# Optimization experiments

Hardware: AMD Instinct MI355X
Metric: run time of the kernel (lower is better)

Reference implementation:

```python
import jax, jax.numpy as jnp
import numpy as np

EPS = 1e-5  # BatchNorm eps (torch default)

def conv2d(x, w, padding=0, dilation=1):
    # x: NCHW, w: OIHW
    return jax.lax.conv_general_dilated(
        x, w, window_strides=(1, 1),
        padding=[(padding, padding), (padding, padding)],
        rhs_dilation=(dilation, dilation),
        dimension_numbers=('NCHW', 'OIHW', 'NCHW'))

def bn_relu(x, scale, bias):
    # eval-mode BatchNorm with running_mean=0, running_var=1, then ReLU
    inv = scale / np.sqrt(1.0 + EPS)
    return jax.nn.relu(x * inv[None, :, None, None] + bias[None, :, None, None])

def setup_inputs() -> dict:
    key = jax.random.key(0)
    ks = jax.random.split(key, 12)
    B, C, H, W = 4, 512, 64, 64
    def nrm(k, shape, fan):
        return jax.random.normal(k, shape, jnp.float32) * np.sqrt(2.0 / fan)
    return {
        'x': jax.random.normal(ks[0], (B, C, H, W), jnp.float32),
        'w_a1': nrm(ks[1], (128, 512, 1, 1), 1 * 1 * 128),
        'w_a2': nrm(ks[2], (128, 512, 3, 3), 3 * 3 * 128),
        'w_a3': nrm(ks[3], (128, 512, 3, 3), 3 * 3 * 128),
        'w_a4': nrm(ks[4], (128, 512, 3, 3), 3 * 3 * 128),
        'w_a5': nrm(ks[5], (128, 512, 1, 1), 1 * 1 * 128),
        'bn_scale': jnp.ones((5, 128), jnp.float32),
        'bn_bias': jnp.zeros((5, 128), jnp.float32),
        'w_q': jax.random.normal(ks[6], (128, 640, 1, 1), jnp.float32) * 0.04,
        'b_q': jnp.zeros((128,), jnp.float32),
        'w_k': jax.random.normal(ks[7], (128, 640, 1, 1), jnp.float32) * 0.04,
        'b_k': jnp.zeros((128,), jnp.float32),
        'w_v': jax.random.normal(ks[8], (512, 512, 1, 1), jnp.float32) * 0.04,
        'b_v': jnp.zeros((512,), jnp.float32),
        'gamma': jax.random.uniform(ks[9], (1,), jnp.float32),
    }

def reference(x, w_a1, w_a2, w_a3, w_a4, w_a5, bn_scale, bn_bias,
              w_q, b_q, w_k, b_k, w_v, b_v, gamma):
    B, C, H, W = x.shape
    N = H * W
    # ASPP branches (query and key paths use identical weights & input,
    # so compute once and reuse — same math as the original)
    b1 = bn_relu(conv2d(x, w_a1, 0, 1), bn_scale[0], bn_bias[0])
    b2 = bn_relu(conv2d(x, w_a2, 2, 2), bn_scale[1], bn_bias[1])
    b3 = bn_relu(conv2d(x, w_a3, 3, 3), bn_scale[2], bn_bias[2])
    b4 = bn_relu(conv2d(x, w_a4, 6, 6), bn_scale[3], bn_bias[3])
    # aspp5: global avg pool -> 1x1 conv -> BN -> ReLU -> bilinear up to HxW
    # (bilinear upsample of a 1x1 map with align_corners=True is a broadcast)
    p5 = jnp.mean(x, axis=(2, 3), keepdims=True)            # [B,512,1,1]
    p5 = bn_relu(conv2d(p5, w_a5, 0, 1), bn_scale[4], bn_bias[4])
    b5 = jnp.broadcast_to(p5, (B, 128, H, W))
    feat = jnp.concatenate([b1, b2, b3, b4, b5], axis=1)    # [B,640,H,W]

    q = (conv2d(feat, w_q) + b_q[None, :, None, None]).reshape(B, 128, N)  # [B,128,N]
    k = (conv2d(feat, w_k) + b_k[None, :, None, None]).reshape(B, 128, N)  # [B,128,N]
    v = (conv2d(x, w_v) + b_v[None, :, None, None]).reshape(B, C, N)       # [B,C,N]

    energy = jnp.einsum('bcn,bcm->bnm', q, k)               # [B,N,N], unscaled
    attention = jax.nn.softmax(energy, axis=-1)
    out = jnp.einsum('bcm,bnm->bcn', v, attention).reshape(B, C, H, W)
    return gamma[0] * out + x
```

## Files before the change

### kernel.cpp

```cpp
#include <hip/hip_runtime.h>

typedef _Float16 f16x8 __attribute__((ext_vector_type(8)));
typedef _Float16 f16x4 __attribute__((ext_vector_type(4)));
typedef float f32x4 __attribute__((ext_vector_type(4)));

#define N_PIX 4096
#define C_IN  512
#define BN_INV 0.99999500003749969f
#define CCH 64

#define GLOAD_LDS16(g, l)                                        \
  __builtin_amdgcn_global_load_lds(                              \
      (const __attribute__((address_space(1))) void*)(g),        \
      (__attribute__((address_space(3))) void*)(l), 16, 0, 0)

__device__ __forceinline__ f32x4 mfma16(f16x8 a, f16x8 b, f32x4 c) {
  return __builtin_amdgcn_mfma_f32_16x16x32_f16(a, b, c, 0, 0, 0);
}
__device__ __forceinline__ f16x8 ldnt(const _Float16* base, int row, int ld, int k0, int lane) {
  return *(const f16x8*)(base + (size_t)(row + (lane & 15)) * ld + k0 + ((lane >> 4) << 3));
}

__global__ __launch_bounds__(256) void k_xT(const float* __restrict__ x, _Float16* __restrict__ xT) {
  __shared__ float t[32][33];
  int b = blockIdx.z, p0 = blockIdx.x * 32, c0 = blockIdx.y * 32;
  int tx = threadIdx.x & 31, ty = threadIdx.x >> 5;
  const float* xb = x + ((size_t)b * C_IN + c0) * N_PIX + p0;
  for (int i = 0; i < 32; i += 8) t[ty + i][tx] = xb[(size_t)(ty + i) * N_PIX + tx];
  __syncthreads();
  _Float16* o = xT + ((size_t)b * N_PIX + p0) * C_IN + c0;
  for (int i = 0; i < 32; i += 8) o[(size_t)(ty + i) * C_IN + tx] = (_Float16)t[tx][ty + i];
}

__global__ __launch_bounds__(256) void k_f2h4(const float* __restrict__ a, _Float16* __restrict__ oa, int na,
                                              const float* __restrict__ b_, _Float16* __restrict__ ob, int nb,
                                              const float* __restrict__ c, _Float16* __restrict__ oc, int nc,
                                              const float* __restrict__ d, _Float16* __restrict__ od, int nd) {
  int i = blockIdx.x * 256 + threadIdx.x;
  if (i < na) { oa[i] = (_Float16)a[i]; return; }
  i -= na;
  if (i < nb) { ob[i] = (_Float16)b_[i]; return; }
  i -= nb;
  if (i < nc) { oc[i] = (_Float16)c[i]; return; }
  i -= nc;
  if (i < nd) od[i] = (_Float16)d[i];
}

__global__ __launch_bounds__(256) void k_packw(const float* __restrict__ w2, const float* __restrict__ w3,
                                               const float* __restrict__ w4, _Float16* __restrict__ wp) {
  int idx = blockIdx.x * 256 + threadIdx.x;
  int conv = idx / 589824;
  int t1 = idx % 589824;
  int tap = t1 / 65536;
  int t2 = t1 % 65536;
  int oc = t2 / 512, c = t2 % 512;
  const float* w = (conv == 0) ? w2 : (conv == 1) ? w3 : w4;
  wp[idx] = (_Float16)w[(size_t)(oc * 512 + c) * 9 + tap];
}

__global__ __launch_bounds__(256) void k_mean(const float* __restrict__ x, float* __restrict__ meanv) {
  int c = blockIdx.x, b = blockIdx.y;
  const float* p = x + ((size_t)b * C_IN + c) * N_PIX;
  float s = 0.f;
  for (int i = threadIdx.x; i < N_PIX; i += 256) s += p[i];
  for (int off = 32; off; off >>= 1) s += __shfl_down(s, off);
  __shared__ float ls[4];
  if ((threadIdx.x & 63) == 0) ls[threadIdx.x >> 6] = s;
  __syncthreads();
  if (threadIdx.x == 0) meanv[(size_t)b * C_IN + c] = (ls[0] + ls[1] + ls[2] + ls[3]) * (1.f / N_PIX);
}

__global__ void k_p5(const float* __restrict__ w5, const float* __restrict__ meanv,
                     const float* __restrict__ bnS, const float* __restrict__ bnB, _Float16* __restrict__ p5h) {
  int b = blockIdx.x, oc = threadIdx.x;
  const float* m = meanv + (size_t)b * C_IN;
  const float* w = w5 + (size_t)oc * C_IN;
  float s = 0.f;
  for (int c = 0; c < C_IN; ++c) s += w[c] * m[c];
  float v = fmaxf(s * bnS[oc] * BN_INV + bnB[oc], 0.f);
  p5h[b * 128 + oc] = (_Float16)v;
}

__global__ __launch_bounds__(256) void k_b5(const _Float16* __restrict__ p5h, _Float16* __restrict__ featT) {
  int i = blockIdx.x * 256 + threadIdx.x;
  int oc = i & 127, p = (i >> 7) & 4095, b = i >> 19;
  featT[((size_t)b * N_PIX + p) * 640 + 512 + oc] = p5h[b * 128 + oc];
}

__global__ __launch_bounds__(256, 4) void k_conv(const _Float16* __restrict__ xT, const _Float16* __restrict__ w1h,
                                                 const _Float16* __restrict__ wph, const float* __restrict__ bnS,
                                                 const float* __restrict__ bnB, _Float16* __restrict__ featT) {
  __shared__ _Float16 Ap[3 * 76 * CCH];
  int y = blockIdx.x;
  int tb = blockIdx.y;
  int task = tb >> 2, b = tb & 3;
  int tid = threadIdx.x, wid = tid >> 6, lane = tid & 63;
  int dil = (task == 0) ? 0 : (task == 1) ? 2 : (task == 2) ? 3 : 6;
  int ntap = task ? 9 : 1;
  int nrow = task ? 3 : 1;
  const _Float16* wt0 = task ? wph + (size_t)(task - 1) * 9 * 128 * C_IN : w1h;
  f32x4 acc[4][2] = {};

  for (int cc = 0; cc < C_IN / CCH; ++cc) {
    int c0 = cc * CCH;
    __syncthreads();
    if (dil) {
      int nz = nrow * 2 * dil * (CCH / 8);
      for (int i = tid; i < nz; i += 256) {
        int cv = (i & (CCH / 8 - 1)) * 8;
        int t2 = i / (CCH / 8);
        int colh = t2 % (2 * dil);
        int r = t2 / (2 * dil);
        int col = (colh < dil) ? colh : 64 + colh;
        int ba = (((r * 76 + col) * CCH + cv) * 2) ^ ((col & 7) << 4);
        *(f16x8*)((char*)Ap + ba) = (f16x8){};
      }
    }
    int nf = nrow * 64 * (CCH / 8);
    for (int i = tid; i < nf; i += 256) {
      int cv = (i & (CCH / 8 - 1)) * 8;
      int t2 = i / (CCH / 8);
      int px = t2 & 63;
      int r = t2 >> 6;
      int ry = y + (r - 1) * dil;
      f16x8 v = {};
      if ((unsigned)ry < 64u)
        v = *(const f16x8*)(xT + ((size_t)b * N_PIX + ry * 64 + px) * C_IN + c0 + cv);
      int col = dil + px;
      int ba = (((r * 76 + col) * CCH + cv) * 2) ^ ((col & 7) << 4);
      *(f16x8*)((char*)Ap + ba) = v;
    }
    __syncthreads();
    for (int tap = 0; tap < ntap; ++tap) {
      int rsel = tap / 3;
      int dx = (tap % 3 - 1) * dil;
      const _Float16* wt = wt0 + (size_t)tap * 128 * C_IN;
#pragma unroll
      for (int k = 0; k < CCH / 32; ++k) {
        f16x8 wf0 = ldnt(wt, wid * 32, C_IN, c0 + k * 32, lane);
        f16x8 wf1 = ldnt(wt, wid * 32 + 16, C_IN, c0 + k * 32, lane);
        f16x8 af[4];
#pragma unroll
        for (int m = 0; m < 4; ++m) {
          int col = dil + dx + m * 16 + (lane & 15);
          int ch = k * 32 + ((lane >> 4) << 3);
          int ba = (((rsel * 76 + col) * CCH + ch) * 2) ^ ((col & 7) << 4);
          af[m] = *(const f16x8*)((char*)Ap + ba);
        }
#pragma unroll
        for (int m = 0; m < 4; ++m) {
          acc[m][0] = mfma16(af[m], wf0, acc[m][0]);
          acc[m][1] = mfma16(af[m], wf1, acc[m][1]);
        }
      }
    }
  }
  int brOff = task * 128;
  _Float16* F = featT + (size_t)b * N_PIX * 640;
#pragma unroll
  for (int n = 0; n < 2; ++n) {
    int oc = wid * 32 + n * 16 + (lane & 15);
    float inv = bnS[brOff + oc] * BN_INV, bs = bnB[brOff + oc];
#pragma unroll
    for (int m = 0; m < 4; ++m) {
#pragma unroll
      for (int r = 0; r < 4; ++r) {
        int pix = y * 64 + m * 16 + ((lane >> 4) << 2) + r;
        F[(size_t)pix * 640 + brOff + oc] = (_Float16)fmaxf(acc[m][n][r] * inv + bs, 0.f);
      }
    }
  }
}

__global__ __launch_bounds__(256) void k_qk(const _Float16* __restrict__ featT, const _Float16* __restrict__ wqh,
                                            const _Float16* __restrict__ wkh, const float* __restrict__ bq,
                                            const float* __restrict__ bk, _Float16* __restrict__ qT,
                                            _Float16* __restrict__ kT) {
  int b = blockIdx.z, which = blockIdx.y, p0 = blockIdx.x * 32;
  const _Float16* wh = which ? wkh : wqh;
  const float* bias = which ? bk : bq;
  _Float16* oT = which ? kT : qT;
  int tid = threadIdx.x, wid = tid >> 6, lane = tid & 63;
  int pw = wid & 1, ocq = wid >> 1;
  const _Float16* A = featT + (size_t)b * N_PIX * 640;
  int pr = p0 + pw * 16;
  f32x4 acc[4] = {};
  for (int kk = 0; kk < 20; ++kk) {
    f16x8 af = ldnt(A, pr, 640, kk * 32, lane);
#pragma unroll
    for (int nn = 0; nn < 4; ++nn) {
      f16x8 bf = ldnt(wh, ocq * 64 + nn * 16, 640, kk * 32, lane);
      acc[nn] = mfma16(af, bf, acc[nn]);
    }
  }
  _Float16* O = oT + (size_t)b * N_PIX * 128;
#pragma unroll
  for (int nn = 0; nn < 4; ++nn) {
    int oc = ocq * 64 + nn * 16 + (lane & 15);
    float bb = bias[oc];
#pragma unroll
    for (int r = 0; r < 4; ++r) {
      int pix = pr + ((lane >> 4) << 2) + r;
      O[(size_t)pix * 128 + oc] = (_Float16)(acc[nn][r] + bb);
    }
  }
}

__global__ __launch_bounds__(256) void k_v(const _Float16* __restrict__ xT, const _Float16* __restrict__ wvh,
                                           const float* __restrict__ bv, _Float16* __restrict__ vv) {
  int b = blockIdx.z, oc0 = blockIdx.x * 64, p0 = blockIdx.y * 128;
  int tid = threadIdx.x, wid = tid >> 6, lane = tid & 63;
  const _Float16* Bm = xT + (size_t)b * N_PIX * C_IN;
  int or0 = oc0 + wid * 16;
  f32x4 acc[8] = {};
  for (int kk = 0; kk < 16; ++kk) {
    f16x8 af = ldnt(wvh, or0, C_IN, kk * 32, lane);
#pragma unroll
    for (int nn = 0; nn < 8; ++nn) {
      f16x8 bf = ldnt(Bm, p0 + nn * 16, C_IN, kk * 32, lane);
      acc[nn] = mfma16(af, bf, acc[nn]);
    }
  }
  _Float16* V = vv + (size_t)b * C_IN * N_PIX;
#pragma unroll
  for (int r = 0; r < 4; ++r) {
    int oc = or0 + ((lane >> 4) << 2) + r;
    float bb = bv[oc];
#pragma unroll
    for (int nn = 0; nn < 8; ++nn) {
      int pix = p0 + nn * 16 + (lane & 15);
      V[(size_t)oc * N_PIX + pix] = (_Float16)(acc[nn][r] + bb);
    }
  }
}

__global__ __launch_bounds__(768, 3) void k_attn(const _Float16* __restrict__ qT, const _Float16* __restrict__ kT,
                                                 const _Float16* __restrict__ vv, const float* __restrict__ x,
                                                 const float* __restrict__ gamma, float* __restrict__ out) {
  __shared__ _Float16 Kb[2][128 * 128];
  __shared__ _Float16 P[2][64 * 128];
  __shared__ float fbuf[2][64];
  __shared__ float sbuf[64];
  int b = blockIdx.y, n0 = blockIdx.x * 64;
  int tid = threadIdx.x, wid = tid >> 6, lane = tid & 63;
  const _Float16* Q = qT + (size_t)b * N_PIX * 128;
  const _Float16* K = kT + (size_t)b * N_PIX * 128;
  const _Float16* V = vv + (size_t)b * C_IN * N_PIX;
  float g = gamma[0];
  f16x8 qf[4];
  int n_local = (wid & 3) * 16 + (lane & 15);
  if (wid < 4) {
#pragma unroll
    for (int kk = 0; kk < 4; ++kk) qf[kk] = ldnt(Q, n0 + wid * 16, 128, kk * 32, lane);
  }
  float m_run = -3.4e38f, sm = 0.f;
  f32x4 acc[4][4];
#pragma unroll
  for (int cc = 0; cc < 4; ++cc)
#pragma unroll
    for (int nn = 0; nn < 4; ++nn) acc[cc][nn] = (f32x4){};

  auto stageK = [&](int it, int buf) {
    const _Float16* src = K + (size_t)it * 128 * 128;
    int cs = (lane & 15) << 4;
#pragma unroll
    for (int i = 0; i < 4; ++i) {
      int rr = wid * 16 + i * 4 + (lane >> 4);
      const char* gp = (const char*)(src + (size_t)rr * 128) + (cs ^ ((rr & 7) << 4));
      char* lp = (char*)&Kb[buf][0] + (size_t)(wid * 16 + i * 4) * 256;
      GLOAD_LDS16(gp, lp);
    }
  };

  auto phaseA = [&](int it) {
    int buf = it & 1;
    const char* kb = (const char*)&Kb[buf][0];
    f32x4 s8[8];
#pragma unroll
    for (int mm = 0; mm < 8; ++mm) {
      int row = mm * 16 + (lane & 15);
      int kboff = (lane >> 4) << 4;
      f32x4 s = {};
#pragma unroll
      for (int kk = 0; kk < 4; ++kk) {
        f16x8 kf = *(const f16x8*)(kb + (size_t)row * 256 + ((kk * 64 + kboff) ^ ((row & 7) << 4)));
        s = mfma16(kf, qf[kk], s);
      }
      s8[mm] = s;
    }
    float tmx = s8[0][0];
#pragma unroll
    for (int mm = 0; mm < 8; ++mm)
      tmx = fmaxf(tmx, fmaxf(fmaxf(s8[mm][0], s8[mm][1]), fmaxf(s8[mm][2], s8[mm][3])));
    tmx = fmaxf(tmx, __shfl_xor(tmx, 16));
    tmx = fmaxf(tmx, __shfl_xor(tmx, 32));
    float f = 1.f;
    if (tmx > m_run + 8.f) {
      f = __expf(m_run - tmx);
      m_run = tmx;
    }
    sm *= f;
    if (lane < 16) fbuf[buf][n_local] = f;
#pragma unroll
    for (int mm = 0; mm < 8; ++mm) {
      f16x4 pv;
#pragma unroll
      for (int r = 0; r < 4; ++r) {
        float p = __expf(s8[mm][r] - m_run);
        sm += p;
        pv[r] = (_Float16)p;
      }
      int m_local = mm * 16 + ((lane >> 4) << 2);
      *(f16x4*)((char*)&P[buf][0] + (size_t)n_local * 256 + ((m_local * 2) ^ ((n_local & 7) << 4))) = pv;
    }
  };

  auto phaseB = [&](int it) {
    int buf = it & 1;
    int c0 = (wid - 4) * 64;
    float f[4];
#pragma unroll
    for (int nn = 0; nn < 4; ++nn) f[nn] = fbuf[buf][nn * 16 + (lane & 15)];
    bool need = (f[0] != 1.f) | (f[1] != 1.f) | (f[2] != 1.f) | (f[3] != 1.f);
    if (__any(need)) {
#pragma unroll
      for (int cc = 0; cc < 4; ++cc)
#pragma unroll
        for (int nn = 0; nn < 4; ++nn) acc[cc][nn] = acc[cc][nn] * f[nn];
    }
#pragma unroll
    for (int k2 = 0; k2 < 4; ++k2) {
      f16x8 pb[4];
#pragma unroll
      for (int nn = 0; nn < 4; ++nn) {
        int n = nn * 16 + (lane & 15);
        int mbyte = k2 * 64 + ((lane >> 4) << 4);
        pb[nn] = *(const f16x8*)((char*)&P[buf][0] + (size_t)n * 256 + (mbyte ^ ((n & 7) << 4)));
      }
      __builtin_amdgcn_s_setprio(1);
#pragma unroll
      for (int cc = 0; cc < 4; ++cc) {
        f16x8 af = ldnt(V, c0 + cc * 16, N_PIX, it * 128 + k2 * 32, lane);
#pragma unroll
        for (int nn = 0; nn < 4; ++nn) acc[cc][nn] = mfma16(af, pb[nn], acc[cc][nn]);
      }
      __builtin_amdgcn_s_setprio(0);
    }
  };

  if (wid < 8) {
    stageK(0, 0);
    stageK(1, 1);
  }
  __syncthreads();
  if (wid < 4) phaseA(0);
  __syncthreads();
  for (int it = 0; it < 32; ++it) {
    if (wid < 8 && it < 30) stageK(it + 2, it & 1);
    if (wid < 4) {
      if (it < 31) phaseA(it + 1);
    } else if (wid >= 4) {
      phaseB(it);
    }
    __syncthreads();
  }

  if (wid < 4) {
    float st = sm;
    st += __shfl_xor(st, 16);
    st += __shfl_xor(st, 32);
    if (lane < 16) sbuf[n_local] = st;
  }
  __syncthreads();
  if (wid >= 4) {
    int c0 = (wid - 4) * 64;
    float inv_s[4];
#pragma unroll
    for (int nn = 0; nn < 4; ++nn) inv_s[nn] = 1.f / sbuf[nn * 16 + (lane & 15)];
#pragma unroll
    for (int cc = 0; cc < 4; ++cc) {
#pragma unroll
      for (int r = 0; r < 4; ++r) {
        int oc = c0 + cc * 16 + ((lane >> 4) << 2) + r;
#pragma unroll
        for (int nn = 0; nn < 4; ++nn) {
          int pix = n0 + nn * 16 + (lane & 15);
          size_t idx = ((size_t)(b * C_IN + oc)) * N_PIX + pix;
          out[idx] = fmaf(g * inv_s[nn], acc[cc][nn][r], x[idx]);
        }
      }
    }
  }
}

extern "C" void kernel_launch(void* const* d_in, const int* in_sizes, int n_in,
                              void* d_out, int out_size, void* d_ws, size_t ws_size,
                              hipStream_t stream) {
  const float* x = (const float*)d_in[0];
  const float* wa1 = (const float*)d_in[1];
  const float* wa2 = (const float*)d_in[2];
  const float* wa3 = (const float*)d_in[3];
  const float* wa4 = (const float*)d_in[4];
  const float* wa5 = (const float*)d_in[5];
  const float* bnS = (const float*)d_in[6];
  const float* bnB = (const float*)d_in[7];
  const float* wq = (const float*)d_in[8];
  const float* bq = (const float*)d_in[9];
  const float* wk = (const float*)d_in[10];
  const float* bk = (const float*)d_in[11];
  const float* wv = (const float*)d_in[12];
  const float* bv = (const float*)d_in[13];
  const float* gamma = (const float*)d_in[14];

  char* ws = (char*)d_ws;
  size_t off = 0;
  auto alloc = [&](size_t bytes) -> char* {
    char* p = ws + off;
    off = (off + bytes + 255) & ~(size_t)255;
    return p;
  };
  _Float16* xT = (_Float16*)alloc((size_t)4 * 4096 * 512 * 2);
  _Float16* featT = (_Float16*)alloc((size_t)4 * 4096 * 640 * 2);
  _Float16* qT = (_Float16*)alloc((size_t)4 * 4096 * 128 * 2);
  _Float16* kT = (_Float16*)alloc((size_t)4 * 4096 * 128 * 2);
  _Float16* vvp = (_Float16*)alloc((size_t)4 * 512 * 4096 * 2);
  _Float16* w1h = (_Float16*)alloc((size_t)128 * 512 * 2);
  _Float16* wph = (_Float16*)alloc((size_t)3 * 9 * 128 * 512 * 2);
  _Float16* wqh = (_Float16*)alloc((size_t)128 * 640 * 2);
  _Float16* wkh = (_Float16*)alloc((size_t)128 * 640 * 2);
  _Float16* wvh = (_Float16*)alloc((size_t)512 * 512 * 2);
  float* meanv = (float*)alloc((size_t)4 * 512 * 4);
  _Float16* p5h = (_Float16*)alloc((size_t)4 * 128 * 2);
  if (off > ws_size) return;

  float* out = (float*)d_out;

  hipLaunchKernelGGL(k_xT, dim3(128, 16, 4), dim3(256), 0, stream, x, xT);
  hipLaunchKernelGGL(k_f2h4, dim3(1920), dim3(256), 0, stream, wa1, w1h, 65536, wq, wqh, 81920, wk, wkh, 81920,
                     wv, wvh, 262144);
  hipLaunchKernelGGL(k_packw, dim3(6912), dim3(256), 0, stream, wa2, wa3, wa4, wph);
  hipLaunchKernelGGL(k_mean, dim3(512, 4), dim3(256), 0, stream, x, meanv);
  hipLaunchKernelGGL(k_p5, dim3(4), dim3(128), 0, stream, wa5, meanv, bnS + 4 * 128, bnB + 4 * 128, p5h);
  hipLaunchKernelGGL(k_b5, dim3(8192), dim3(256), 0, stream, p5h, featT);
  hipLaunchKernelGGL(k_conv, dim3(64, 16), dim3(256), 0, stream, xT, w1h, wph, bnS, bnB, featT);
  hipLaunchKernelGGL(k_qk, dim3(128, 2, 4), dim3(256), 0, stream, featT, wqh, wkh, bq, bk, qT, kT);
  hipLaunchKernelGGL(k_v, dim3(8, 32, 4), dim3(256), 0, stream, xT, wvh, bv, vvp);
  hipLaunchKernelGGL(k_attn, dim3(64, 4), dim3(768), 0, stream, qT, kT, vvp, x, gamma, out);
}
```

Measured before the change: 421.2 us.

## Fold constant pooled branch into per-batch q/k bias and swizzle block order

The pooled ASPP branch is constant over pixels, so its contribution to q and k is folded into a per-batch bias computed in k_p5. This removes the broadcast kernel, shrinks featT from 640 to 512 channels, and cuts the q/k reduction from 20 to 16 k-steps. Separately, conv, v and attention grids are flattened and their block indices swizzled so that neighbouring blocks land on different XCDs. The conv tap loop is also fully unrolled for the dilated tasks, which may raise register pressure.

```diff
diff --git a/kernel.cpp b/kernel.cpp
--- a/kernel.cpp
+++ b/kernel.cpp
@@ -32,18 +32,18 @@
   for (int i = 0; i < 32; i += 8) o[(size_t)(ty + i) * C_IN + tx] = (_Float16)t[tx][ty + i];
 }
 
-__global__ __launch_bounds__(256) void k_f2h4(const float* __restrict__ a, _Float16* __restrict__ oa, int na,
-                                              const float* __restrict__ b_, _Float16* __restrict__ ob, int nb,
-                                              const float* __restrict__ c, _Float16* __restrict__ oc, int nc,
-                                              const float* __restrict__ d, _Float16* __restrict__ od, int nd) {
+__global__ __launch_bounds__(256) void k_f2hx(const float* __restrict__ wa1, _Float16* __restrict__ w1h,
+                                              const float* __restrict__ wv, _Float16* __restrict__ wvh,
+                                              const float* __restrict__ wq, _Float16* __restrict__ wqh,
+                                              const float* __restrict__ wk, _Float16* __restrict__ wkh) {
   int i = blockIdx.x * 256 + threadIdx.x;
-  if (i < na) { oa[i] = (_Float16)a[i]; return; }
-  i -= na;
-  if (i < nb) { ob[i] = (_Float16)b_[i]; return; }
-  i -= nb;
-  if (i < nc) { oc[i] = (_Float16)c[i]; return; }
-  i -= nc;
-  if (i < nd) od[i] = (_Float16)d[i];
+  if (i < 65536) { w1h[i] = (_Float16)wa1[i]; return; }
+  i -= 65536;
+  if (i < 262144) { wvh[i] = (_Float16)wv[i]; return; }
+  i -= 262144;
+  if (i < 65536) { int oc = i >> 9, c = i & 511; wqh[i] = (_Float16)wq[oc * 640 + c]; return; }
+  i -= 65536;
+  if (i < 65536) { int oc = i >> 9, c = i & 511; wkh[i] = (_Float16)wk[oc * 640 + c]; }
 }
 
 __global__ __launch_bounds__(256) void k_packw(const float* __restrict__ w2, const float* __restrict__ w3,
@@ -71,32 +71,39 @@
 }
 
 __global__ void k_p5(const float* __restrict__ w5, const float* __restrict__ meanv,
-                     const float* __restrict__ bnS, const float* __restrict__ bnB, _Float16* __restrict__ p5h) {
+                     const float* __restrict__ bnS, const float* __restrict__ bnB,
+                     const float* __restrict__ wq, const float* __restrict__ bq,
+                     const float* __restrict__ wk, const float* __restrict__ bk,
+                     float* __restrict__ bq2, float* __restrict__ bk2) {
+  __shared__ float p5s[128];
   int b = blockIdx.x, oc = threadIdx.x;
   const float* m = meanv + (size_t)b * C_IN;
   const float* w = w5 + (size_t)oc * C_IN;
   float s = 0.f;
   for (int c = 0; c < C_IN; ++c) s += w[c] * m[c];
-  float v = fmaxf(s * bnS[oc] * BN_INV + bnB[oc], 0.f);
-  p5h[b * 128 + oc] = (_Float16)v;
-}
-
-__global__ __launch_bounds__(256) void k_b5(const _Float16* __restrict__ p5h, _Float16* __restrict__ featT) {
-  int i = blockIdx.x * 256 + threadIdx.x;
-  int oc = i & 127, p = (i >> 7) & 4095, b = i >> 19;
-  featT[((size_t)b * N_PIX + p) * 640 + 512 + oc] = p5h[b * 128 + oc];
+  p5s[oc] = fmaxf(s * bnS[oc] * BN_INV + bnB[oc], 0.f);
+  __syncthreads();
+  float aq = bq[oc], ak = bk[oc];
+  for (int c = 0; c < 128; ++c) {
+    float pv = p5s[c];
+    aq += wq[oc * 640 + 512 + c] * pv;
+    ak += wk[oc * 640 + 512 + c] * pv;
+  }
+  bq2[b * 128 + oc] = aq;
+  bk2[b * 128 + oc] = ak;
 }
 
 __global__ __launch_bounds__(256, 4) void k_conv(const _Float16* __restrict__ xT, const _Float16* __restrict__ w1h,
                                                  const _Float16* __restrict__ wph, const float* __restrict__ bnS,
                                                  const float* __restrict__ bnB, _Float16* __restrict__ featT) {
   __shared__ _Float16 Ap[3 * 76 * CCH];
-  int y = blockIdx.x;
-  int tb = blockIdx.y;
+  int bid = blockIdx.x;
+  int swz = (bid & 7) * 128 + (bid >> 3);
+  int y = swz & 63;
+  int tb = swz >> 6;
   int task = tb >> 2, b = tb & 3;
   int tid = threadIdx.x, wid = tid >> 6, lane = tid & 63;
   int dil = (task == 0) ? 0 : (task == 1) ? 2 : (task == 2) ? 3 : 6;
-  int ntap = task ? 9 : 1;
   int nrow = task ? 3 : 1;
   const _Float16* wt0 = task ? wph + (size_t)(task - 1) * 9 * 128 * C_IN : w1h;
   f32x4 acc[4][2] = {};
@@ -131,10 +138,7 @@
       *(f16x8*)((char*)Ap + ba) = v;
     }
     __syncthreads();
-    for (int tap = 0; tap < ntap; ++tap) {
-      int rsel = tap / 3;
-      int dx = (tap % 3 - 1) * dil;
-      const _Float16* wt = wt0 + (size_t)tap * 128 * C_IN;
+    auto do_tap = [&](int rsel, int dx, const _Float16* wt) {
 #pragma unroll
       for (int k = 0; k < CCH / 32; ++k) {
         f16x8 wf0 = ldnt(wt, wid * 32, C_IN, c0 + k * 32, lane);
@@ -153,10 +157,17 @@
           acc[m][1] = mfma16(af[m], wf1, acc[m][1]);
         }
       }
+    };
+    if (task == 0) {
+      do_tap(0, 0, wt0);
+    } else {
+#pragma unroll
+      for (int tap = 0; tap < 9; ++tap)
+        do_tap(tap / 3, (tap % 3 - 1) * dil, wt0 + (size_t)tap * 128 * C_IN);
     }
   }
   int brOff = task * 128;
-  _Float16* F = featT + (size_t)b * N_PIX * 640;
+  _Float16* F = featT + (size_t)b * N_PIX * 512;
 #pragma unroll
   for (int n = 0; n < 2; ++n) {
     int oc = wid * 32 + n * 16 + (lane & 15);
@@ -166,30 +177,30 @@
 #pragma unroll
       for (int r = 0; r < 4; ++r) {
         int pix = y * 64 + m * 16 + ((lane >> 4) << 2) + r;
-        F[(size_t)pix * 640 + brOff + oc] = (_Float16)fmaxf(acc[m][n][r] * inv + bs, 0.f);
+        F[(size_t)pix * 512 + brOff + oc] = (_Float16)fmaxf(acc[m][n][r] * inv + bs, 0.f);
       }
     }
   }
 }
 
 __global__ __launch_bounds__(256) void k_qk(const _Float16* __restrict__ featT, const _Float16* __restrict__ wqh,
-                                            const _Float16* __restrict__ wkh, const float* __restrict__ bq,
-                                            const float* __restrict__ bk, _Float16* __restrict__ qT,
+                                            const _Float16* __restrict__ wkh, const float* __restrict__ bq2,
+                                            const float* __restrict__ bk2, _Float16* __restrict__ qT,
                                             _Float16* __restrict__ kT) {
   int b = blockIdx.z, which = blockIdx.y, p0 = blockIdx.x * 32;
   const _Float16* wh = which ? wkh : wqh;
-  const float* bias = which ? bk : bq;
+  const float* bias = (which ? bk2 : bq2) + b * 128;
   _Float16* oT = which ? kT : qT;
   int tid = threadIdx.x, wid = tid >> 6, lane = tid & 63;
   int pw = wid & 1, ocq = wid >> 1;
-  const _Float16* A = featT + (size_t)b * N_PIX * 640;
+  const _Float16* A = featT + (size_t)b * N_PIX * 512;
   int pr = p0 + pw * 16;
   f32x4 acc[4] = {};
-  for (int kk = 0; kk < 20; ++kk) {
-    f16x8 af = ldnt(A, pr, 640, kk * 32, lane);
+  for (int kk = 0; kk < 16; ++kk) {
+    f16x8 af = ldnt(A, pr, 512, kk * 32, lane);
 #pragma unroll
     for (int nn = 0; nn < 4; ++nn) {
-      f16x8 bf = ldnt(wh, ocq * 64 + nn * 16, 640, kk * 32, lane);
+      f16x8 bf = ldnt(wh, ocq * 64 + nn * 16, 512, kk * 32, lane);
       acc[nn] = mfma16(af, bf, acc[nn]);
     }
   }
@@ -208,7 +219,11 @@
 
 __global__ __launch_bounds__(256) void k_v(const _Float16* __restrict__ xT, const _Float16* __restrict__ wvh,
                                            const float* __restrict__ bv, _Float16* __restrict__ vv) {
-  int b = blockIdx.z, oc0 = blockIdx.x * 64, p0 = blockIdx.y * 128;
+  int bid = blockIdx.x;
+  int swz = (bid & 7) * 128 + (bid >> 3);
+  int oc0 = (swz & 7) * 64;
+  int p0 = ((swz >> 3) & 31) * 128;
+  int b = swz >> 8;
   int tid = threadIdx.x, wid = tid >> 6, lane = tid & 63;
   const _Float16* Bm = xT + (size_t)b * N_PIX * C_IN;
   int or0 = oc0 + wid * 16;
@@ -241,7 +256,10 @@
   __shared__ _Float16 P[2][64 * 128];
   __shared__ float fbuf[2][64];
   __shared__ float sbuf[64];
-  int b = blockIdx.y, n0 = blockIdx.x * 64;
+  int bid = blockIdx.x;
+  int swz = (bid & 7) * 32 + (bid >> 3);
+  int n0 = (swz & 63) * 64;
+  int b = swz >> 6;
   int tid = threadIdx.x, wid = tid >> 6, lane = tid & 63;
   const _Float16* Q = qT + (size_t)b * N_PIX * 128;
   const _Float16* K = kT + (size_t)b * N_PIX * 128;
@@ -359,7 +377,7 @@
     if (wid < 8 && it < 30) stageK(it + 2, it & 1);
     if (wid < 4) {
       if (it < 31) phaseA(it + 1);
-    } else if (wid >= 4) {
+    } else {
       phaseB(it);
     }
     __syncthreads();
@@ -420,30 +438,30 @@
     return p;
   };
   _Float16* xT = (_Float16*)alloc((size_t)4 * 4096 * 512 * 2);
-  _Float16* featT = (_Float16*)alloc((size_t)4 * 4096 * 640 * 2);
+  _Float16* featT = (_Float16*)alloc((size_t)4 * 4096 * 512 * 2);
   _Float16* qT = (_Float16*)alloc((size_t)4 * 4096 * 128 * 2);
   _Float16* kT = (_Float16*)alloc((size_t)4 * 4096 * 128 * 2);
   _Float16* vvp = (_Float16*)alloc((size_t)4 * 512 * 4096 * 2);
   _Float16* w1h = (_Float16*)alloc((size_t)128 * 512 * 2);
   _Float16* wph = (_Float16*)alloc((size_t)3 * 9 * 128 * 512 * 2);
-  _Float16* wqh = (_Float16*)alloc((size_t)128 * 640 * 2);
-  _Float16* wkh = (_Float16*)alloc((size_t)128 * 640 * 2);
+  _Float16* wqh = (_Float16*)alloc((size_t)128 * 512 * 2);
+  _Float16* wkh = (_Float16*)alloc((size_t)128 * 512 * 2);
   _Float16* wvh = (_Float16*)alloc((size_t)512 * 512 * 2);
   float* meanv = (float*)alloc((size_t)4 * 512 * 4);
-  _Float16* p5h = (_Float16*)alloc((size_t)4 * 128 * 2);
+  float* bq2 = (float*)alloc((size_t)4 * 128 * 4);
+  float* bk2 = (float*)alloc((size_t)4 * 128 * 4);
   if (off > ws_size) return;
 
   float* out = (float*)d_out;
 
   hipLaunchKernelGGL(k_xT, dim3(128, 16, 4), dim3(256), 0, stream, x, xT);
-  hipLaunchKernelGGL(k_f2h4, dim3(1920), dim3(256), 0, stream, wa1, w1h, 65536, wq, wqh, 81920, wk, wkh, 81920,
-                     wv, wvh, 262144);
+  hipLaunchKernelGGL(k_f2hx, dim3(1792), dim3(256), 0, stream, wa1, w1h, wv, wvh, wq, wqh, wk, wkh);
   hipLaunchKernelGGL(k_packw, dim3(6912), dim3(256), 0, stream, wa2, wa3, wa4, wph);
   hipLaunchKernelGGL(k_mean, dim3(512, 4), dim3(256), 0, stream, x, meanv);
-  hipLaunchKernelGGL(k_p5, dim3(4), dim3(128), 0, stream, wa5, meanv, bnS + 4 * 128, bnB + 4 * 128, p5h);
-  hipLaunchKernelGGL(k_b5, dim3(8192), dim3(256), 0, stream, p5h, featT);
-  hipLaunchKernelGGL(k_conv, dim3(64, 16), dim3(256), 0, stream, xT, w1h, wph, bnS, bnB, featT);
-  hipLaunchKernelGGL(k_qk, dim3(128, 2, 4), dim3(256), 0, stream, featT, wqh, wkh, bq, bk, qT, kT);
-  hipLaunchKernelGGL(k_v, dim3(8, 32, 4), dim3(256), 0, stream, xT, wvh, bv, vvp);
-  hipLaunchKernelGGL(k_attn, dim3(64, 4), dim3(768), 0, stream, qT, kT, vvp, x, gamma, out);
-}
+  hipLaunchKernelGGL(k_p5, dim3(4), dim3(128), 0, stream, wa5, meanv, bnS + 4 * 128, bnB + 4 * 128,
+                     wq, bq, wk, bk, bq2, bk2);
+  hipLaunchKernelGGL(k_conv, dim3(1024), dim3(256), 0, stream, xT, w1h, wph, bnS, bnB, featT);
+  hipLaunchKernelGGL(k_qk, dim3(128, 2, 4), dim3(256), 0, stream, featT, wqh, wkh, bq2, bk2, qT, kT);
+  hipLaunchKernelGGL(k_v, dim3(1024), dim3(256), 0, stream, xT, wvh, bv, vvp);
+  hipLaunchKernelGGL(k_attn, dim3(256), dim3(768), 0, stream, qT, kT, vvp, x, gamma, out);
+}
```

Result: slower. 532.4 us (+26.4%).
